# Kernel optimization log

Measured on AMD Instinct MI355X. Metric: run time of the kernel, lower is better.

Reference implementation:

```python
import jax, jax.numpy as jnp
import numpy as np

THRESHOLD = 0.5
DILATION_ITERS = 5  # scipy binary_dilation(iterations=5)


def _dilate_cross(mask, iters=DILATION_ITERS):
    # mask: [T, H, W] bool. scipy's default 3D structure on a [H,W,1] frame
    # degenerates to a 2D 4-connected (cross) structuring element.
    # One iteration = OR of center and the 4 axis-aligned neighbors.
    for _ in range(iters):
        p = jnp.pad(mask, ((0, 0), (1, 1), (1, 1)))
        mask = (p[:, 1:-1, 1:-1]
                | p[:, :-2, 1:-1] | p[:, 2:, 1:-1]
                | p[:, 1:-1, :-2] | p[:, 1:-1, 2:])
    return mask


def setup_inputs() -> dict:
    key = jax.random.key(0)
    k1, k2 = jax.random.split(key)
    X = jax.random.normal(k1, (3, 128, 256, 256), dtype=jnp.float32)          # [C,T,H,W]
    background = jax.random.normal(k2, (256, 256, 3), dtype=jnp.float32)      # [H,W,C]
    return {"X": X, "background": background}


def reference(X, background):
    Xp = jnp.transpose(X, (1, 2, 3, 0))                                       # [T,H,W,C]
    mask = jnp.sum(jnp.abs(Xp - background), axis=-1) > THRESHOLD             # [T,H,W]
    mask = _dilate_cross(mask)
    out = Xp * mask[..., None].astype(Xp.dtype)
    return jnp.transpose(out, (3, 0, 1, 2))                                   # [C,T,H,W]
```

## Files before the change

kernel.cpp:

```cpp
#include <hip/hip_runtime.h>
#include <stdint.h>

#define TT 128
#define HH 256
#define WW 256
#define PLANE (TT*HH*WW)
#define FRAME (HH*WW)
#define ROWS 32
#define TPF  (HH/ROWS)
#define REPEAT 2
#define GROUPS (TPF/REPEAT)
#define HALO 5
#define BROWS (ROWS + 2*HALO)
#define THRESH 0.5f

typedef float nfloat4 __attribute__((ext_vector_type(4)));

__device__ __forceinline__ uint64_t shfl64(uint64_t v, int src) {
    uint32_t lo = (uint32_t)v, hi = (uint32_t)(v >> 32);
    lo = __shfl(lo, src);
    hi = __shfl(hi, src);
    return ((uint64_t)hi << 32) | lo;
}

__device__ __forceinline__ uint64_t pack16(uint32_t nib) {
    int lane = threadIdx.x & 63;
    uint64_t v = (uint64_t)nib << (4 * (lane & 15));
    v |= __shfl_xor(v, 1);
    v |= __shfl_xor(v, 2);
    v |= __shfl_xor(v, 4);
    v |= __shfl_xor(v, 8);
    return v;
}

__device__ __forceinline__ uint32_t nib_from(nfloat4 x0, nfloat4 x1, nfloat4 x2,
                                             const float* __restrict__ bg,
                                             int gr, int col4) {
    const nfloat4* bp = (const nfloat4*)(bg + ((size_t)gr * WW + 4 * col4) * 3);
    nfloat4 q0 = bp[0], q1 = bp[1], q2 = bp[2];
    uint32_t nib = 0;
    nib |= ((fabsf(x0[0] - q0[0]) + fabsf(x1[0] - q0[1]) + fabsf(x2[0] - q0[2])) > THRESH) ? 1u : 0u;
    nib |= ((fabsf(x0[1] - q0[3]) + fabsf(x1[1] - q1[0]) + fabsf(x2[1] - q1[1])) > THRESH) ? 2u : 0u;
    nib |= ((fabsf(x0[2] - q1[2]) + fabsf(x1[2] - q1[3]) + fabsf(x2[2] - q2[0])) > THRESH) ? 4u : 0u;
    nib |= ((fabsf(x0[3] - q2[1]) + fabsf(x1[3] - q2[2]) + fabsf(x2[3] - q2[3])) > THRESH) ? 8u : 0u;
    return nib;
}

__global__ __launch_bounds__(512) void fused_kernel(const float* __restrict__ X,
                                                    const float* __restrict__ bg,
                                                    float* __restrict__ out) {
    __shared__ uint64_t mbuf[2][BROWS][4];
    const int t    = blockIdx.x >> 2;
    const int j0   = (blockIdx.x & (GROUPS - 1)) * REPEAT;
    const int tid  = threadIdx.x;
    const int lane = tid & 63;
    const int wave = tid >> 6;
    const int col4 = lane;

#pragma unroll
    for (int rep = 0; rep < REPEAT; ++rep) {
        const int r0 = (j0 + rep) * ROWS;
        uint64_t (*B)[4] = mbuf[rep & 1];

        nfloat4 xv[4][3];
#pragma unroll
        for (int k = 0; k < 4; ++k) {
            const int gr = r0 + wave + 8 * k;
            size_t pix = (size_t)t * FRAME + (size_t)gr * WW + 4 * col4;
            xv[k][0] = *(const nfloat4*)(X + pix);
            xv[k][1] = *(const nfloat4*)(X + (size_t)PLANE + pix);
            xv[k][2] = *(const nfloat4*)(X + 2 * (size_t)PLANE + pix);
        }
        const int slotA = wave;
        const int grA   = (slotA < 5) ? (r0 - HALO + slotA) : (r0 + ROWS + (slotA - 5));
        const int browA = (slotA < 5) ? slotA : (HALO + ROWS + (slotA - 5));
        const bool okA  = (grA >= 0) && (grA < HH);
        nfloat4 ha0 = 0, ha1 = 0, ha2 = 0;
        if (okA) {
            size_t pix = (size_t)t * FRAME + (size_t)grA * WW + 4 * col4;
            ha0 = *(const nfloat4*)(X + pix);
            ha1 = *(const nfloat4*)(X + (size_t)PLANE + pix);
            ha2 = *(const nfloat4*)(X + 2 * (size_t)PLANE + pix);
        }
        const int grB   = r0 + ROWS + 3 + wave;
        const int browB = HALO + ROWS + 3 + wave;
        const bool okB  = (wave < 2) && (grB < HH);
        nfloat4 hb0 = 0, hb1 = 0, hb2 = 0;
        if (okB) {
            size_t pix = (size_t)t * FRAME + (size_t)grB * WW + 4 * col4;
            hb0 = *(const nfloat4*)(X + pix);
            hb1 = *(const nfloat4*)(X + (size_t)PLANE + pix);
            hb2 = *(const nfloat4*)(X + 2 * (size_t)PLANE + pix);
        }

#pragma unroll
        for (int k = 0; k < 4; ++k) {
            const int gr = r0 + wave + 8 * k;
            uint64_t w = pack16(nib_from(xv[k][0], xv[k][1], xv[k][2], bg, gr, col4));
            if ((lane & 15) == 0) B[HALO + wave + 8 * k][lane >> 4] = w;
        }
        {
            uint32_t nb = okA ? nib_from(ha0, ha1, ha2, bg, grA, col4) : 0u;
            uint64_t w = pack16(nb);
            if ((lane & 15) == 0) B[browA][lane >> 4] = w;
        }
        if (wave < 2) {
            uint32_t nb = okB ? nib_from(hb0, hb1, hb2, bg, grB, col4) : 0u;
            uint64_t w = pack16(nb);
            if ((lane & 15) == 0) B[browB][lane >> 4] = w;
        }
        __syncthreads();

        if (wave == 0) {
            uint64_t r_[4];
#pragma unroll
            for (int i = 0; i < 4; ++i) r_[i] = (lane < BROWS) ? B[lane][i] : 0ULL;
#pragma unroll
            for (int it = 0; it < 5; ++it) {
                uint64_t nr[4];
#pragma unroll
                for (int i = 0; i < 4; ++i) {
                    uint64_t c  = r_[i];
                    uint64_t l  = (i > 0) ? r_[i - 1] : 0ULL;
                    uint64_t rr = (i < 3) ? r_[i + 1] : 0ULL;
                    uint64_t u  = shfl64(c, lane - 1);
                    uint64_t d  = shfl64(c, lane + 1);
                    u = (lane == 0) ? 0ULL : u;
                    nr[i] = c | (c << 1) | (l >> 63) | (c >> 1) | (rr << 63) | u | d;
                }
#pragma unroll
                for (int i = 0; i < 4; ++i) r_[i] = nr[i];
            }
            if (lane >= HALO && lane < HALO + ROWS) {
#pragma unroll
                for (int i = 0; i < 4; ++i) B[lane][i] = r_[i];
            }
        }
        __syncthreads();

#pragma unroll
        for (int k = 0; k < 4; ++k) {
            const int row = wave + 8 * k;
            uint64_t w = B[HALO + row][col4 >> 4];
            uint32_t nb = (uint32_t)(w >> (4 * (col4 & 15))) & 0xFu;
            float m0 = (float)(nb & 1u);
            float m1 = (float)((nb >> 1) & 1u);
            float m2 = (float)((nb >> 2) & 1u);
            float m3 = (float)((nb >> 3) & 1u);
            size_t pix = (size_t)t * FRAME + (size_t)(r0 + row) * WW + 4 * col4;
#pragma unroll
            for (int c = 0; c < 3; ++c) {
                nfloat4 v = xv[k][c];
                nfloat4 nv = { v[0] * m0, v[1] * m1, v[2] * m2, v[3] * m3 };
                __builtin_nontemporal_store(nv, (nfloat4*)(out + (size_t)c * PLANE + pix));
            }
        }
    }
}

extern "C" void kernel_launch(void* const* d_in, const int* in_sizes, int n_in,
                              void* d_out, int out_size, void* d_ws, size_t ws_size,
                              hipStream_t stream) {
    const float* X  = (const float*)d_in[0];
    const float* bg = (const float*)d_in[1];
    float* out = (float*)d_out;
    const int nblocks = TT * GROUPS;
    fused_kernel<<<nblocks, 512, 0, stream>>>(X, bg, out);
}
```

Before: 40.75 us.

## One tile per block, XCD-aware remap, redundant per-wave dilation via shuffles

Drops the two-tile REPEAT loop so each block handles a single 32-row tile, which doubles the grid, and remaps block IDs so neighbouring tiles of a frame land on the same XCD. Every wave now runs the 5-iteration bit dilation itself, and the dilated mask is handed to the output stage with cross-lane shuffles instead of a second shared-memory write and barrier. The shared buffer row is padded to 5 words to reduce bank conflicts. This removes one barrier and the serial single-wave dilation phase, at the cost of redundant dilation work in all waves and more blocks to launch.

```diff
diff --git a/kernel.cpp b/kernel.cpp
--- a/kernel.cpp
+++ b/kernel.cpp
@@ -7,12 +7,10 @@
 #define PLANE (TT*HH*WW)
 #define FRAME (HH*WW)
 #define ROWS 32
-#define TPF  (HH/ROWS)
-#define REPEAT 2
-#define GROUPS (TPF/REPEAT)
 #define HALO 5
 #define BROWS (ROWS + 2*HALO)
 #define THRESH 0.5f
+#define NXCD 8
 
 typedef float nfloat4 __attribute__((ext_vector_type(4)));
 
@@ -49,111 +47,104 @@
 __global__ __launch_bounds__(512) void fused_kernel(const float* __restrict__ X,
                                                     const float* __restrict__ bg,
                                                     float* __restrict__ out) {
-    __shared__ uint64_t mbuf[2][BROWS][4];
-    const int t    = blockIdx.x >> 2;
-    const int j0   = (blockIdx.x & (GROUPS - 1)) * REPEAT;
+    __shared__ uint64_t B[BROWS][5];
+    const int wg   = (int)(blockIdx.x % NXCD) * ((TT * 8) / NXCD) + (int)(blockIdx.x / NXCD);
+    const int t    = wg >> 3;
+    const int j    = wg & 7;
+    const int r0   = j * ROWS;
     const int tid  = threadIdx.x;
     const int lane = tid & 63;
     const int wave = tid >> 6;
     const int col4 = lane;
 
+    const int slotA = wave;
+    const int grA   = (slotA < 5) ? (r0 - HALO + slotA) : (r0 + ROWS + (slotA - 5));
+    const int browA = (slotA < 5) ? slotA : (HALO + ROWS + (slotA - 5));
+    const bool okA  = (grA >= 0) && (grA < HH);
+    nfloat4 ha0 = 0, ha1 = 0, ha2 = 0;
+    if (okA) {
+        size_t pix = (size_t)t * FRAME + (size_t)grA * WW + 4 * col4;
+        ha0 = *(const nfloat4*)(X + pix);
+        ha1 = *(const nfloat4*)(X + (size_t)PLANE + pix);
+        ha2 = *(const nfloat4*)(X + 2 * (size_t)PLANE + pix);
+    }
+    const int grB   = r0 + ROWS + 3 + wave;
+    const int browB = HALO + ROWS + 3 + wave;
+    const bool okB  = (wave < 2) && (grB < HH);
+    nfloat4 hb0 = 0, hb1 = 0, hb2 = 0;
+    if (okB) {
+        size_t pix = (size_t)t * FRAME + (size_t)grB * WW + 4 * col4;
+        hb0 = *(const nfloat4*)(X + pix);
+        hb1 = *(const nfloat4*)(X + (size_t)PLANE + pix);
+        hb2 = *(const nfloat4*)(X + 2 * (size_t)PLANE + pix);
+    }
+
+    nfloat4 xv[4][3];
 #pragma unroll
-    for (int rep = 0; rep < REPEAT; ++rep) {
-        const int r0 = (j0 + rep) * ROWS;
-        uint64_t (*B)[4] = mbuf[rep & 1];
+    for (int k = 0; k < 4; ++k) {
+        const int gr = r0 + wave + 8 * k;
+        size_t pix = (size_t)t * FRAME + (size_t)gr * WW + 4 * col4;
+        xv[k][0] = *(const nfloat4*)(X + pix);
+        xv[k][1] = *(const nfloat4*)(X + (size_t)PLANE + pix);
+        xv[k][2] = *(const nfloat4*)(X + 2 * (size_t)PLANE + pix);
+        uint64_t w = pack16(nib_from(xv[k][0], xv[k][1], xv[k][2], bg, gr, col4));
+        if ((lane & 15) == 0) B[HALO + wave + 8 * k][lane >> 4] = w;
+    }
+    {
+        uint32_t nb = okA ? nib_from(ha0, ha1, ha2, bg, grA, col4) : 0u;
+        uint64_t w = pack16(nb);
+        if ((lane & 15) == 0) B[browA][lane >> 4] = w;
+    }
+    if (wave < 2) {
+        uint32_t nb = okB ? nib_from(hb0, hb1, hb2, bg, grB, col4) : 0u;
+        uint64_t w = pack16(nb);
+        if ((lane & 15) == 0) B[browB][lane >> 4] = w;
+    }
+    __syncthreads();
 
-        nfloat4 xv[4][3];
+    uint64_t r_[4];
 #pragma unroll
-        for (int k = 0; k < 4; ++k) {
-            const int gr = r0 + wave + 8 * k;
-            size_t pix = (size_t)t * FRAME + (size_t)gr * WW + 4 * col4;
-            xv[k][0] = *(const nfloat4*)(X + pix);
-            xv[k][1] = *(const nfloat4*)(X + (size_t)PLANE + pix);
-            xv[k][2] = *(const nfloat4*)(X + 2 * (size_t)PLANE + pix);
+    for (int i = 0; i < 4; ++i) r_[i] = (lane < BROWS) ? B[lane][i] : 0ULL;
+#pragma unroll
+    for (int it = 0; it < 5; ++it) {
+        uint64_t nr[4];
+#pragma unroll
+        for (int i = 0; i < 4; ++i) {
+            uint64_t c  = r_[i];
+            uint64_t l  = (i > 0) ? r_[i - 1] : 0ULL;
+            uint64_t rr = (i < 3) ? r_[i + 1] : 0ULL;
+            uint64_t u  = shfl64(c, lane - 1);
+            uint64_t d  = shfl64(c, lane + 1);
+            u = (lane == 0) ? 0ULL : u;
+            nr[i] = c | (c << 1) | (l >> 63) | (c >> 1) | (rr << 63) | u | d;
         }
-        const int slotA = wave;
-        const int grA   = (slotA < 5) ? (r0 - HALO + slotA) : (r0 + ROWS + (slotA - 5));
-        const int browA = (slotA < 5) ? slotA : (HALO + ROWS + (slotA - 5));
-        const bool okA  = (grA >= 0) && (grA < HH);
-        nfloat4 ha0 = 0, ha1 = 0, ha2 = 0;
-        if (okA) {
-            size_t pix = (size_t)t * FRAME + (size_t)grA * WW + 4 * col4;
-            ha0 = *(const nfloat4*)(X + pix);
-            ha1 = *(const nfloat4*)(X + (size_t)PLANE + pix);
-            ha2 = *(const nfloat4*)(X + 2 * (size_t)PLANE + pix);
-        }
-        const int grB   = r0 + ROWS + 3 + wave;
-        const int browB = HALO + ROWS + 3 + wave;
-        const bool okB  = (wave < 2) && (grB < HH);
-        nfloat4 hb0 = 0, hb1 = 0, hb2 = 0;
-        if (okB) {
-            size_t pix = (size_t)t * FRAME + (size_t)grB * WW + 4 * col4;
-            hb0 = *(const nfloat4*)(X + pix);
-            hb1 = *(const nfloat4*)(X + (size_t)PLANE + pix);
-            hb2 = *(const nfloat4*)(X + 2 * (size_t)PLANE + pix);
-        }
+#pragma unroll
+        for (int i = 0; i < 4; ++i) r_[i] = nr[i];
+    }
 
 #pragma unroll
-        for (int k = 0; k < 4; ++k) {
-            const int gr = r0 + wave + 8 * k;
-            uint64_t w = pack16(nib_from(xv[k][0], xv[k][1], xv[k][2], bg, gr, col4));
-            if ((lane & 15) == 0) B[HALO + wave + 8 * k][lane >> 4] = w;
-        }
-        {
-            uint32_t nb = okA ? nib_from(ha0, ha1, ha2, bg, grA, col4) : 0u;
-            uint64_t w = pack16(nb);
-            if ((lane & 15) == 0) B[browA][lane >> 4] = w;
-        }
-        if (wave < 2) {
-            uint32_t nb = okB ? nib_from(hb0, hb1, hb2, bg, grB, col4) : 0u;
-            uint64_t w = pack16(nb);
-            if ((lane & 15) == 0) B[browB][lane >> 4] = w;
-        }
-        __syncthreads();
-
-        if (wave == 0) {
-            uint64_t r_[4];
+    for (int k = 0; k < 4; ++k) {
+        const int row = wave + 8 * k;
+        const int src = HALO + row;
+        uint64_t t0 = shfl64(r_[0], src);
+        uint64_t t1 = shfl64(r_[1], src);
+        uint64_t t2 = shfl64(r_[2], src);
+        uint64_t t3 = shfl64(r_[3], src);
+        const int idx = col4 >> 4;
+        uint64_t lo = (idx & 1) ? t1 : t0;
+        uint64_t hi = (idx & 1) ? t3 : t2;
+        uint64_t w  = (idx & 2) ? hi : lo;
+        uint32_t nb = (uint32_t)(w >> (4 * (col4 & 15))) & 0xFu;
+        float m0 = (float)(nb & 1u);
+        float m1 = (float)((nb >> 1) & 1u);
+        float m2 = (float)((nb >> 2) & 1u);
+        float m3 = (float)((nb >> 3) & 1u);
+        size_t pix = (size_t)t * FRAME + (size_t)(r0 + row) * WW + 4 * col4;
 #pragma unroll
-            for (int i = 0; i < 4; ++i) r_[i] = (lane < BROWS) ? B[lane][i] : 0ULL;
-#pragma unroll
-            for (int it = 0; it < 5; ++it) {
-                uint64_t nr[4];
-#pragma unroll
-                for (int i = 0; i < 4; ++i) {
-                    uint64_t c  = r_[i];
-                    uint64_t l  = (i > 0) ? r_[i - 1] : 0ULL;
-                    uint64_t rr = (i < 3) ? r_[i + 1] : 0ULL;
-                    uint64_t u  = shfl64(c, lane - 1);
-                    uint64_t d  = shfl64(c, lane + 1);
-                    u = (lane == 0) ? 0ULL : u;
-                    nr[i] = c | (c << 1) | (l >> 63) | (c >> 1) | (rr << 63) | u | d;
-                }
-#pragma unroll
-                for (int i = 0; i < 4; ++i) r_[i] = nr[i];
-            }
-            if (lane >= HALO && lane < HALO + ROWS) {
-#pragma unroll
-                for (int i = 0; i < 4; ++i) B[lane][i] = r_[i];
-            }
-        }
-        __syncthreads();
-
-#pragma unroll
-        for (int k = 0; k < 4; ++k) {
-            const int row = wave + 8 * k;
-            uint64_t w = B[HALO + row][col4 >> 4];
-            uint32_t nb = (uint32_t)(w >> (4 * (col4 & 15))) & 0xFu;
-            float m0 = (float)(nb & 1u);
-            float m1 = (float)((nb >> 1) & 1u);
-            float m2 = (float)((nb >> 2) & 1u);
-            float m3 = (float)((nb >> 3) & 1u);
-            size_t pix = (size_t)t * FRAME + (size_t)(r0 + row) * WW + 4 * col4;
-#pragma unroll
-            for (int c = 0; c < 3; ++c) {
-                nfloat4 v = xv[k][c];
-                nfloat4 nv = { v[0] * m0, v[1] * m1, v[2] * m2, v[3] * m3 };
-                __builtin_nontemporal_store(nv, (nfloat4*)(out + (size_t)c * PLANE + pix));
-            }
+        for (int c = 0; c < 3; ++c) {
+            nfloat4 v = xv[k][c];
+            nfloat4 nv = { v[0] * m0, v[1] * m1, v[2] * m2, v[3] * m3 };
+            __builtin_nontemporal_store(nv, (nfloat4*)(out + (size_t)c * PLANE + pix));
         }
     }
 }
@@ -164,6 +155,6 @@
     const float* X  = (const float*)d_in[0];
     const float* bg = (const float*)d_in[1];
     float* out = (float*)d_out;
-    const int nblocks = TT * GROUPS;
+    const int nblocks = TT * (HH / ROWS);
     fused_kernel<<<nblocks, 512, 0, stream>>>(X, bg, out);
 }
```

Result: slower. 44.83 us (+10.0%).
